# Kernel optimization log

Hardware: AMD Instinct MI355X
Metric: run time of the kernel (lower is better)

## Reference

```python
import jax, jax.numpy as jnp
import numpy as np

DIM = 768
NUM_HEADS = 12
SMALLEST_RATIO = 0.25
LARGEST_RATIO = 1.0


def setup_inputs() -> dict:
    key = jax.random.key(0)
    k0, k1, k2 = jax.random.split(key, 3)
    B, N = 4, 2048
    x = jax.random.normal(k0, (B, N, DIM), dtype=jnp.float32)
    Wqkv = jax.random.normal(k1, (3 * DIM, DIM), dtype=jnp.float32) * 0.02
    bqkv = jnp.zeros((3 * DIM,), dtype=jnp.float32)
    Wproj = jax.random.normal(k2, (DIM, DIM), dtype=jnp.float32) * 0.02
    bproj = jnp.zeros((DIM,), dtype=jnp.float32)
    return {"x": x, "Wqkv": Wqkv, "bqkv": bqkv, "Wproj": Wproj, "bproj": bproj, "ratio": 1}


def reference(x, Wqkv, bqkv, Wproj, bproj, ratio):
    dc = int(ratio * DIM)
    # dynamic slimmable-width slicing: smallest/largest ratio take leading block,
    # intermediate ratios take trailing block
    if ratio == SMALLEST_RATIO or ratio == LARGEST_RATIO:
        wq, bq = Wqkv[: dc * 3, :dc], bqkv[: dc * 3]
        wp, bp = Wproj[:dc, :dc], bproj[:dc]
    else:
        wq, bq = Wqkv[-dc * 3 :, -dc:], bqkv[-dc * 3 :]
        wp, bp = Wproj[-dc:, -dc:], bproj[-dc:]
    B, N, C = x.shape
    hd = C // NUM_HEADS
    scale = (DIM // NUM_HEADS) ** -0.5  # set at init from full dim, not sliced C
    qkv = x @ wq.T + bq                               # [B, N, 3C]
    qkv = qkv.reshape(B, N, 3, NUM_HEADS, hd).transpose(2, 0, 3, 1, 4)  # [3,B,H,N,hd]
    q, k, v = qkv[0], qkv[1], qkv[2]
    attn = jax.nn.softmax(jnp.einsum("bhqd,bhkd->bhqk", q, k) * scale, axis=-1)
    out = jnp.einsum("bhqk,bhkd->bhqd", attn, v)      # [B,H,N,hd]
    out = out.transpose(0, 2, 1, 3).reshape(B, N, C)
    return out @ wp.T + bp
```

## Files before the change

### kernel.cpp

```cpp
#include <hip/hip_runtime.h>

typedef __bf16 bf16x8 __attribute__((ext_vector_type(8)));
typedef __bf16 bf16x2 __attribute__((ext_vector_type(2)));
typedef float  f32x4  __attribute__((ext_vector_type(4)));
typedef float  f32x16 __attribute__((ext_vector_type(16)));
typedef unsigned short u16;
typedef unsigned u32x2 __attribute__((ext_vector_type(2)));
typedef unsigned u32x4 __attribute__((ext_vector_type(4)));

__device__ __forceinline__ u16 f2bf(float f) {
  return __builtin_bit_cast(u16, (__bf16)f);
}
__device__ __forceinline__ unsigned pack2(float lo, float hi) {
  bf16x2 t;
  t[0] = (__bf16)lo; t[1] = (__bf16)hi;
  return __builtin_bit_cast(unsigned, t);
}

#define GLOAD16(g, l) __builtin_amdgcn_global_load_lds( \
    (__attribute__((address_space(1))) void*)(void*)(g), \
    (__attribute__((address_space(3))) void*)(l), 16, 0, 0)

#define QSCALE 0.18033688011112042f

__global__ __launch_bounds__(256) void cvt_all(
    const float* __restrict__ x, const float* __restrict__ wq,
    const float* __restrict__ wp, unsigned* __restrict__ xb,
    unsigned* __restrict__ wqb, unsigned* __restrict__ wpb) {
  int i = blockIdx.x * 256 + threadIdx.x;
  const float* src;
  unsigned* dst;
  if (i < 786432) {
    src = x; dst = xb;
  } else if (i < 786432 + 221184) {
    src = wq; dst = wqb; i -= 786432;
  } else {
    src = wp; dst = wpb; i -= 786432 + 221184;
  }
  const float4* s = (const float4*)src + 2 * (size_t)i;
  float4 a = s[0], b = s[1];
  u32x4 o = {pack2(a.x, a.y), pack2(a.z, a.w), pack2(b.x, b.y), pack2(b.z, b.w)};
  *((u32x4*)dst + i) = o;
}

template<int EPI>
__global__ __launch_bounds__(256) void gemm_tn(
    const u16* __restrict__ A, const u16* __restrict__ B,
    const float* __restrict__ bias, float* __restrict__ outF,
    u16* __restrict__ qws, u16* __restrict__ kws, u16* __restrict__ vtws,
    int M, int N, int K) {
  __shared__ __align__(16) u16 As[8192];
  __shared__ __align__(16) u16 Bs[8192];
  const int tid = threadIdx.x;
  const int ln = tid & 63, wv = tid >> 6;
  const int wr = wv >> 1, wc = wv & 1;
  const int m0 = blockIdx.x * 128, n0 = blockIdx.y * 128;

  f32x4 acc[4][4] = {};

  const int c0 = tid, c1 = tid + 256;
  const int r0 = c0 >> 2, kc0 = ((c0 & 3) ^ ((r0 >> 1) & 3)) * 8;
  const int r1 = c1 >> 2, kc1 = ((c1 & 3) ^ ((r1 >> 1) & 3)) * 8;
  const u16* ag0 = A + (size_t)(m0 + r0) * K + kc0;
  const u16* ag1 = A + (size_t)(m0 + r1) * K + kc1;
  const u16* bg0 = B + (size_t)(n0 + r0) * K + kc0;
  const u16* bg1 = B + (size_t)(n0 + r1) * K + kc1;

  GLOAD16(ag0, As + wv * 512);
  GLOAD16(ag1, As + 2048 + wv * 512);
  GLOAD16(bg0, Bs + wv * 512);
  GLOAD16(bg1, Bs + 2048 + wv * 512);
  __syncthreads();

  int cur = 0;
  for (int k0 = 0; k0 < K; k0 += 32) {
    const int nxt = cur ^ 1;
    if (k0 + 32 < K) {
      GLOAD16(ag0 + k0 + 32, As + nxt * 4096 + wv * 512);
      GLOAD16(ag1 + k0 + 32, As + nxt * 4096 + 2048 + wv * 512);
      GLOAD16(bg0 + k0 + 32, Bs + nxt * 4096 + wv * 512);
      GLOAD16(bg1 + k0 + 32, Bs + nxt * 4096 + 2048 + wv * 512);
    }
    const u16* ab = As + cur * 4096;
    const u16* bb = Bs + cur * 4096;
    bf16x8 af[4], bfr[4];
#pragma unroll
    for (int i = 0; i < 4; ++i) {
      int ra = wr * 64 + i * 16 + (ln & 15);
      af[i] = *(const bf16x8*)(ab + ra * 32 + (((ln >> 4) ^ ((ra >> 1) & 3)) * 8));
      int rb = wc * 64 + i * 16 + (ln & 15);
      bfr[i] = *(const bf16x8*)(bb + rb * 32 + (((ln >> 4) ^ ((rb >> 1) & 3)) * 8));
    }
#pragma unroll
    for (int i = 0; i < 4; ++i)
#pragma unroll
      for (int j = 0; j < 4; ++j)
        acc[i][j] = __builtin_amdgcn_mfma_f32_16x16x32_bf16(af[i], bfr[j], acc[i][j], 0, 0, 0);
    __syncthreads();
    cur = nxt;
  }

  if (EPI == 1) {
#pragma unroll
    for (int j = 0; j < 4; ++j) {
      int col = n0 + wc * 64 + j * 16 + (ln & 15);
      float bj = bias[col];
#pragma unroll
      for (int i = 0; i < 4; ++i) {
        int mr = m0 + wr * 64 + i * 16 + ((ln >> 4) << 2);
#pragma unroll
        for (int r = 0; r < 4; ++r)
          outF[(size_t)(mr + r) * N + col] = acc[i][j][r] + bj;
      }
    }
  } else {
    const int s = n0 / 768;
#pragma unroll
    for (int j = 0; j < 4; ++j) {
      int col = n0 + wc * 64 + j * 16 + (ln & 15);
      float bj = bias[col];
      int ns = col - s * 768;
      int h = ns >> 6, d = ns & 63;
#pragma unroll
      for (int i = 0; i < 4; ++i) {
        int m = m0 + wr * 64 + i * 16 + ((ln >> 4) << 2);
        int b = m >> 11, iseq = m & 2047;
        size_t bh = (size_t)(b * 12 + h);
        if (s == 0) {
#pragma unroll
          for (int r = 0; r < 4; ++r)
            qws[(bh * 2048 + iseq + r) * 64 + d] = f2bf((acc[i][j][r] + bj) * QSCALE);
        } else if (s == 1) {
#pragma unroll
          for (int r = 0; r < 4; ++r)
            kws[(bh * 2048 + iseq + r) * 64 + d] = f2bf(acc[i][j][r] + bj);
        } else {
          u32x2 pk = {pack2(acc[i][j][0] + bj, acc[i][j][1] + bj),
                      pack2(acc[i][j][2] + bj, acc[i][j][3] + bj)};
          *(u32x2*)(vtws + ((size_t)bh * 64 + (iseq >> 5)) * 2048 +
                    ((iseq >> 3) & 3) * 512 + (size_t)d * 8 + (iseq & 7)) = pk;
        }
      }
    }
  }
}

#define SWZ(v) (((v) & 32) | (((v) & 31) ^ (ln & 31)))
__global__ __launch_bounds__(256, 3) void attn_fa(
    const u16* __restrict__ qws, const u16* __restrict__ kws,
    const u16* __restrict__ vtws, u16* __restrict__ aows) {
  __shared__ __align__(16) u16 SM[16384];
  __shared__ float Ls[256];
  const int tid = threadIdx.x, ln = tid & 63, wv = tid >> 6;
  const int lq = ln & 31, hi = ln >> 5;
  const int qw = wv & 1;
  const int p  = wv >> 1;

  const int flat = blockIdx.y * 16 + blockIdx.x;
  const int xcd = flat & 7, jj = flat >> 3;
  const int bh = xcd * 6 + (jj % 6);
  const int q0 = (jj / 6) * 128 + qw * 64;

  const int kv0 = p * 1024;
  const size_t kbase = (size_t)bh * 2048 * 64;

  bf16x8 qf[2][4];
#pragma unroll
  for (int g = 0; g < 2; ++g) {
    const u16* qp = qws + kbase + (size_t)(q0 + g * 32 + lq) * 64 + hi * 8;
#pragma unroll
    for (int dc = 0; dc < 4; ++dc) qf[g][dc] = *(const bf16x8*)(qp + dc * 16);
  }

  const f32x16 zc = {};
  f32x16 o0[2] = {}, o1[2] = {};
  float lsum[2] = {0.f, 0.f};

  int koff[4], voff[2];
#pragma unroll
  for (int dc = 0; dc < 4; ++dc)
    koff[dc] = lq * 64 + (((dc * 2 + hi) ^ (lq & 7)) * 8);
#pragma unroll
  for (int c = 0; c < 2; ++c)
    voff[c] = (c * 2 + hi) * 512 + lq * 8;

  const int s0i = qw * 128 + ln, s1i = s0i + 64;
  const int kvA = s0i >> 3, kvB = s1i >> 3;
  const int piA = (kvA & ~12) | ((kvA & 4) << 1) | ((kvA & 8) >> 1);
  const int piB = (kvB & ~12) | ((kvB & 4) << 1) | ((kvB & 8) >> 1);
  const u16* kg0 = kws + kbase + (size_t)(kv0 + piA) * 64 + (((s0i & 7) ^ (kvA & 7)) * 8);
  const u16* kg1 = kws + kbase + (size_t)(kv0 + piB) * 64 + (((s1i & 7) ^ (kvB & 7)) * 8);
  const u16* vg  = vtws + ((size_t)bh * 64 + (kv0 >> 5)) * 2048 + s0i * 8;
  u16* Kb = SM + p * 4096;
  u16* Vb = SM + 8192 + p * 4096;
  const int sd = qw * 1024;

#define STAGE(buf, t) do { \
    GLOAD16(kg0 + (size_t)(t) * 2048, Kb + (buf) * 2048 + sd); \
    GLOAD16(kg1 + (size_t)(t) * 2048, Kb + (buf) * 2048 + sd + 512); \
    GLOAD16(vg + (size_t)(t) * 2048, Vb + (buf) * 2048 + sd); \
    GLOAD16(vg + (size_t)(t) * 2048 + 512, Vb + (buf) * 2048 + sd + 512); \
  } while (0)

  STAGE(0, 0);
  __syncthreads();

  int cur = 0;
  for (int it = 0; it < 32; ++it) {
    const int nxt = cur ^ 1;
    if (it + 1 < 32) STAGE(nxt, it + 1);
    const u16* kbuf = Kb + cur * 2048;
    const u16* vbuf = Vb + cur * 2048;

    f32x16 s[2];
    {
      bf16x8 kf = *(const bf16x8*)(kbuf + koff[0]);
      s[0] = __builtin_amdgcn_mfma_f32_32x32x16_bf16(kf, qf[0][0], zc, 0, 0, 0);
      s[1] = __builtin_amdgcn_mfma_f32_32x32x16_bf16(kf, qf[1][0], zc, 0, 0, 0);
    }
#pragma unroll
    for (int dc = 1; dc < 4; ++dc) {
      bf16x8 kf = *(const bf16x8*)(kbuf + koff[dc]);
      s[0] = __builtin_amdgcn_mfma_f32_32x32x16_bf16(kf, qf[0][dc], s[0], 0, 0, 0);
      s[1] = __builtin_amdgcn_mfma_f32_32x32x16_bf16(kf, qf[1][dc], s[1], 0, 0, 0);
    }

#pragma unroll
    for (int g = 0; g < 2; ++g) {
      float a = 0.f;
#pragma unroll
      for (int r = 0; r < 16; ++r) {
        float e = __builtin_amdgcn_exp2f(s[g][r]); s[g][r] = e; a += e;
      }
      lsum[g] += a;
    }

#pragma unroll
    for (int c = 0; c < 2; ++c) {
      bf16x8 va = *(const bf16x8*)(vbuf + voff[c]);
      bf16x8 vb2 = *(const bf16x8*)(vbuf + voff[c] + 256);
#pragma unroll
      for (int g = 0; g < 2; ++g) {
        const int base = c * 8;
        u32x4 pw = {pack2(s[g][base + 0], s[g][base + 1]),
                    pack2(s[g][base + 2], s[g][base + 3]),
                    pack2(s[g][base + 4], s[g][base + 5]),
                    pack2(s[g][base + 6], s[g][base + 7])};
        bf16x8 pfrag = __builtin_bit_cast(bf16x8, pw);
        o0[g] = __builtin_amdgcn_mfma_f32_32x32x16_bf16(va, pfrag, o0[g], 0, 0, 0);
        o1[g] = __builtin_amdgcn_mfma_f32_32x32x16_bf16(vb2, pfrag, o1[g], 0, 0, 0);
      }
    }
    __syncthreads();
    cur = nxt;
  }
#undef STAGE

  float lg[2];
#pragma unroll
  for (int g = 0; g < 2; ++g) {
    lg[g] = lsum[g];
    lg[g] += __shfl_xor(lg[g], 32);
  }

  float* exO = (float*)SM + qw * 4096 + ln * 64;
  if (p == 1) {
#pragma unroll
    for (int r = 0; r < 16; ++r) {
      exO[SWZ(r)]      = o0[0][r];
      exO[SWZ(16 + r)] = o1[0][r];
      exO[SWZ(32 + r)] = o0[1][r];
      exO[SWZ(48 + r)] = o1[1][r];
    }
    Ls[qw * 128 + ln * 2 + 0] = lg[0];
    Ls[qw * 128 + ln * 2 + 1] = lg[1];
  }
  __syncthreads();
  if (p == 0) {
#pragma unroll
    for (int r = 0; r < 16; ++r) {
      o0[0][r] += exO[SWZ(r)];
      o1[0][r] += exO[SWZ(16 + r)];
      o0[1][r] += exO[SWZ(32 + r)];
      o1[1][r] += exO[SWZ(48 + r)];
    }
    lg[0] += Ls[qw * 128 + ln * 2 + 0];
    lg[1] += Ls[qw * 128 + ln * 2 + 1];

    const int b = bh / 12, h = bh % 12;
#pragma unroll
    for (int g = 0; g < 2; ++g) {
      const float rl = 1.0f / lg[g];
      u16* orow = aows + (size_t)(b * 2048 + q0 + g * 32 + lq) * 768 + h * 64;
#pragma unroll
      for (int t = 0; t < 4; ++t) {
        u32x2 pk0 = {pack2(o0[g][4 * t + 0] * rl, o0[g][4 * t + 1] * rl),
                     pack2(o0[g][4 * t + 2] * rl, o0[g][4 * t + 3] * rl)};
        u32x2 pk1 = {pack2(o1[g][4 * t + 0] * rl, o1[g][4 * t + 1] * rl),
                     pack2(o1[g][4 * t + 2] * rl, o1[g][4 * t + 3] * rl)};
        *(u32x2*)(orow + t * 8 + 4 * hi)      = pk0;
        *(u32x2*)(orow + 32 + t * 8 + 4 * hi) = pk1;
      }
    }
  }
}

extern "C" void kernel_launch(void* const* d_in, const int* in_sizes, int n_in,
                              void* d_out, int out_size, void* d_ws, size_t ws_size,
                              hipStream_t stream) {
  const float* x     = (const float*)d_in[0];
  const float* Wqkv  = (const float*)d_in[1];
  const float* bqkv  = (const float*)d_in[2];
  const float* Wproj = (const float*)d_in[3];
  const float* bproj = (const float*)d_in[4];
  float* out = (float*)d_out;

  u16* xb   = (u16*)d_ws;
  u16* wqb  = xb  + 6291456;
  u16* wpb  = wqb + 1769472;
  u16* qws  = wpb + 589824;
  u16* kws  = qws + 6291456;
  u16* vtws = kws + 6291456;
  u16* aows = vtws + 6291456;

  cvt_all<<<4224, 256, 0, stream>>>(x, Wqkv, Wproj,
                                    (unsigned*)xb, (unsigned*)wqb, (unsigned*)wpb);

  gemm_tn<0><<<dim3(64, 18), 256, 0, stream>>>(xb, wqb, bqkv, nullptr,
                                               qws, kws, vtws, 8192, 2304, 768);
  attn_fa<<<dim3(16, 48), 256, 0, stream>>>(qws, kws, vtws, aows);
  gemm_tn<1><<<dim3(64, 6), 256, 0, stream>>>(aows, wpb, bproj, out,
                                              nullptr, nullptr, nullptr,
                                              8192, 768, 768);
}
```

Before: 136.5 us.

## Halve attention query tile per wave and double grid for occupancy

Each wave in the attention kernel now processes 32 query rows instead of 64, so the block covers 64 queries and the grid doubles to 1536 blocks. Register use for accumulators, Q fragments and scores drops, and launch bounds go from 3 to 4 blocks per CU. The cross-wave reduction buffer is simplified to a strided, unswizzled layout. The exp sum is split into two partial accumulators. In exchange, K/V tiles are loaded twice as often per query, which doubles LDS and global traffic for K/V, and the unswizzled reduction layout may cause bank conflicts.

```diff
diff --git a/kernel.cpp b/kernel.cpp
--- a/kernel.cpp
+++ b/kernel.cpp
@@ -145,36 +145,33 @@
   }
 }
 
-#define SWZ(v) (((v) & 32) | (((v) & 31) ^ (ln & 31)))
-__global__ __launch_bounds__(256, 3) void attn_fa(
+__global__ __launch_bounds__(256, 4) void attn_fa(
     const u16* __restrict__ qws, const u16* __restrict__ kws,
     const u16* __restrict__ vtws, u16* __restrict__ aows) {
   __shared__ __align__(16) u16 SM[16384];
-  __shared__ float Ls[256];
   const int tid = threadIdx.x, ln = tid & 63, wv = tid >> 6;
   const int lq = ln & 31, hi = ln >> 5;
   const int qw = wv & 1;
   const int p  = wv >> 1;
 
-  const int flat = blockIdx.y * 16 + blockIdx.x;
+  const int flat = blockIdx.y * 32 + blockIdx.x;
   const int xcd = flat & 7, jj = flat >> 3;
   const int bh = xcd * 6 + (jj % 6);
-  const int q0 = (jj / 6) * 128 + qw * 64;
+  const int q0 = (jj / 6) * 64 + qw * 32;
 
   const int kv0 = p * 1024;
   const size_t kbase = (size_t)bh * 2048 * 64;
 
-  bf16x8 qf[2][4];
-#pragma unroll
-  for (int g = 0; g < 2; ++g) {
-    const u16* qp = qws + kbase + (size_t)(q0 + g * 32 + lq) * 64 + hi * 8;
-#pragma unroll
-    for (int dc = 0; dc < 4; ++dc) qf[g][dc] = *(const bf16x8*)(qp + dc * 16);
+  bf16x8 qf[4];
+  {
+    const u16* qp = qws + kbase + (size_t)(q0 + lq) * 64 + hi * 8;
+#pragma unroll
+    for (int dc = 0; dc < 4; ++dc) qf[dc] = *(const bf16x8*)(qp + dc * 16);
   }
 
   const f32x16 zc = {};
-  f32x16 o0[2] = {}, o1[2] = {};
-  float lsum[2] = {0.f, 0.f};
+  f32x16 o0 = {}, o1 = {};
+  float lsum = 0.f;
 
   int koff[4], voff[2];
 #pragma unroll
@@ -212,95 +209,74 @@
     const u16* kbuf = Kb + cur * 2048;
     const u16* vbuf = Vb + cur * 2048;
 
-    f32x16 s[2];
+    f32x16 s;
     {
       bf16x8 kf = *(const bf16x8*)(kbuf + koff[0]);
-      s[0] = __builtin_amdgcn_mfma_f32_32x32x16_bf16(kf, qf[0][0], zc, 0, 0, 0);
-      s[1] = __builtin_amdgcn_mfma_f32_32x32x16_bf16(kf, qf[1][0], zc, 0, 0, 0);
+      s = __builtin_amdgcn_mfma_f32_32x32x16_bf16(kf, qf[0], zc, 0, 0, 0);
     }
 #pragma unroll
     for (int dc = 1; dc < 4; ++dc) {
       bf16x8 kf = *(const bf16x8*)(kbuf + koff[dc]);
-      s[0] = __builtin_amdgcn_mfma_f32_32x32x16_bf16(kf, qf[0][dc], s[0], 0, 0, 0);
-      s[1] = __builtin_amdgcn_mfma_f32_32x32x16_bf16(kf, qf[1][dc], s[1], 0, 0, 0);
-    }
-
-#pragma unroll
-    for (int g = 0; g < 2; ++g) {
-      float a = 0.f;
-#pragma unroll
-      for (int r = 0; r < 16; ++r) {
-        float e = __builtin_amdgcn_exp2f(s[g][r]); s[g][r] = e; a += e;
-      }
-      lsum[g] += a;
-    }
+      s = __builtin_amdgcn_mfma_f32_32x32x16_bf16(kf, qf[dc], s, 0, 0, 0);
+    }
+
+    float a = 0.f, b2 = 0.f;
+#pragma unroll
+    for (int r = 0; r < 16; r += 2) {
+      float e0 = __builtin_amdgcn_exp2f(s[r]);     s[r] = e0;     a  += e0;
+      float e1 = __builtin_amdgcn_exp2f(s[r + 1]); s[r + 1] = e1; b2 += e1;
+    }
+    lsum += a + b2;
 
 #pragma unroll
     for (int c = 0; c < 2; ++c) {
       bf16x8 va = *(const bf16x8*)(vbuf + voff[c]);
       bf16x8 vb2 = *(const bf16x8*)(vbuf + voff[c] + 256);
-#pragma unroll
-      for (int g = 0; g < 2; ++g) {
-        const int base = c * 8;
-        u32x4 pw = {pack2(s[g][base + 0], s[g][base + 1]),
-                    pack2(s[g][base + 2], s[g][base + 3]),
-                    pack2(s[g][base + 4], s[g][base + 5]),
-                    pack2(s[g][base + 6], s[g][base + 7])};
-        bf16x8 pfrag = __builtin_bit_cast(bf16x8, pw);
-        o0[g] = __builtin_amdgcn_mfma_f32_32x32x16_bf16(va, pfrag, o0[g], 0, 0, 0);
-        o1[g] = __builtin_amdgcn_mfma_f32_32x32x16_bf16(vb2, pfrag, o1[g], 0, 0, 0);
-      }
+      const int base = c * 8;
+      u32x4 pw = {pack2(s[base + 0], s[base + 1]),
+                  pack2(s[base + 2], s[base + 3]),
+                  pack2(s[base + 4], s[base + 5]),
+                  pack2(s[base + 6], s[base + 7])};
+      bf16x8 pfrag = __builtin_bit_cast(bf16x8, pw);
+      o0 = __builtin_amdgcn_mfma_f32_32x32x16_bf16(va, pfrag, o0, 0, 0, 0);
+      o1 = __builtin_amdgcn_mfma_f32_32x32x16_bf16(vb2, pfrag, o1, 0, 0, 0);
     }
     __syncthreads();
     cur = nxt;
   }
 #undef STAGE
 
-  float lg[2];
-#pragma unroll
-  for (int g = 0; g < 2; ++g) {
-    lg[g] = lsum[g];
-    lg[g] += __shfl_xor(lg[g], 32);
-  }
-
-  float* exO = (float*)SM + qw * 4096 + ln * 64;
+  float lg = lsum + __shfl_xor(lsum, 32);
+
+  float* ex = (float*)SM + qw * 2048 + ln;
   if (p == 1) {
 #pragma unroll
     for (int r = 0; r < 16; ++r) {
-      exO[SWZ(r)]      = o0[0][r];
-      exO[SWZ(16 + r)] = o1[0][r];
-      exO[SWZ(32 + r)] = o0[1][r];
-      exO[SWZ(48 + r)] = o1[1][r];
-    }
-    Ls[qw * 128 + ln * 2 + 0] = lg[0];
-    Ls[qw * 128 + ln * 2 + 1] = lg[1];
+      ex[r * 64]        = o0[r];
+      ex[(16 + r) * 64] = o1[r];
+    }
+    ((float*)SM)[4096 + qw * 64 + ln] = lg;
   }
   __syncthreads();
   if (p == 0) {
 #pragma unroll
     for (int r = 0; r < 16; ++r) {
-      o0[0][r] += exO[SWZ(r)];
-      o1[0][r] += exO[SWZ(16 + r)];
-      o0[1][r] += exO[SWZ(32 + r)];
-      o1[1][r] += exO[SWZ(48 + r)];
-    }
-    lg[0] += Ls[qw * 128 + ln * 2 + 0];
-    lg[1] += Ls[qw * 128 + ln * 2 + 1];
-
+      o0[r] += ex[r * 64];
+      o1[r] += ex[(16 + r) * 64];
+    }
+    lg += ((float*)SM)[4096 + qw * 64 + ln];
+
+    const float rl = 1.0f / lg;
     const int b = bh / 12, h = bh % 12;
-#pragma unroll
-    for (int g = 0; g < 2; ++g) {
-      const float rl = 1.0f / lg[g];
-      u16* orow = aows + (size_t)(b * 2048 + q0 + g * 32 + lq) * 768 + h * 64;
-#pragma unroll
-      for (int t = 0; t < 4; ++t) {
-        u32x2 pk0 = {pack2(o0[g][4 * t + 0] * rl, o0[g][4 * t + 1] * rl),
-                     pack2(o0[g][4 * t + 2] * rl, o0[g][4 * t + 3] * rl)};
-        u32x2 pk1 = {pack2(o1[g][4 * t + 0] * rl, o1[g][4 * t + 1] * rl),
-                     pack2(o1[g][4 * t + 2] * rl, o1[g][4 * t + 3] * rl)};
-        *(u32x2*)(orow + t * 8 + 4 * hi)      = pk0;
-        *(u32x2*)(orow + 32 + t * 8 + 4 * hi) = pk1;
-      }
+    u16* orow = aows + (size_t)(b * 2048 + q0 + lq) * 768 + h * 64;
+#pragma unroll
+    for (int t2 = 0; t2 < 4; ++t2) {
+      u32x2 pk0 = {pack2(o0[4 * t2 + 0] * rl, o0[4 * t2 + 1] * rl),
+                   pack2(o0[4 * t2 + 2] * rl, o0[4 * t2 + 3] * rl)};
+      u32x2 pk1 = {pack2(o1[4 * t2 + 0] * rl, o1[4 * t2 + 1] * rl),
+                   pack2(o1[4 * t2 + 2] * rl, o1[4 * t2 + 3] * rl)};
+      *(u32x2*)(orow + t2 * 8 + 4 * hi)      = pk0;
+      *(u32x2*)(orow + 32 + t2 * 8 + 4 * hi) = pk1;
     }
   }
 }
@@ -328,7 +304,7 @@
 
   gemm_tn<0><<<dim3(64, 18), 256, 0, stream>>>(xb, wqb, bqkv, nullptr,
                                                qws, kws, vtws, 8192, 2304, 768);
-  attn_fa<<<dim3(16, 48), 256, 0, stream>>>(qws, kws, vtws, aows);
+  attn_fa<<<dim3(32, 48), 256, 0, stream>>>(qws, kws, vtws, aows);
   gemm_tn<1><<<dim3(64, 6), 256, 0, stream>>>(aows, wpb, bproj, out,
                                               nullptr, nullptr, nullptr,
                                               8192, 768, 768);
```

Result: slower. 144.7 us (+6.0%).
